# Kernel tuning notes

Hardware: AMD Instinct MI355X
Metric: run time of the kernel (lower is better)

Reference implementation:

```python
import jax, jax.numpy as jnp
import numpy as np

N_NODES = 100000
N_EDGES = 1600000
D_IN, D_HID, D_OUT = 128, 128, 64


def setup_inputs() -> dict:
    key = jax.random.key(0)
    ks = jax.random.split(key, 6)
    x = jax.random.normal(ks[0], (N_NODES, D_IN), dtype=jnp.float32)
    edge_index = jax.random.randint(ks[1], (2, N_EDGES), 0, N_NODES, dtype=jnp.int64)
    s1 = 1.0 / np.sqrt(D_IN)
    s2 = 1.0 / np.sqrt(D_HID)
    return {
        "x": x,
        "edge_index": edge_index,
        "Wl1": jax.random.uniform(ks[2], (D_HID, D_IN), jnp.float32, -s1, s1),
        "bl1": jnp.zeros((D_HID,), jnp.float32),
        "Wr1": jax.random.uniform(ks[3], (D_HID, D_IN), jnp.float32, -s1, s1),
        "Wl2": jax.random.uniform(ks[4], (D_OUT, D_HID), jnp.float32, -s2, s2),
        "bl2": jnp.zeros((D_OUT,), jnp.float32),
        "Wr2": jax.random.uniform(ks[5], (D_OUT, D_HID), jnp.float32, -s2, s2),
    }


def _sage_conv(x, src, dst, Wl, bl, Wr, n_nodes):
    # mean-aggregate neighbor features src -> dst
    agg = jax.ops.segment_sum(x[src], dst, num_segments=n_nodes)  # [N, d_in]
    deg = jax.ops.segment_sum(jnp.ones((src.shape[0],), x.dtype), dst, num_segments=n_nodes)
    agg = agg / jnp.maximum(deg, 1.0)[:, None]
    # PyG SAGEConv: lin_l(agg) + lin_r(x), bias only on lin_l
    return agg @ Wl.T + bl + x @ Wr.T


def reference(x, edge_index, Wl1, bl1, Wr1, Wl2, bl2, Wr2):
    src, dst = edge_index[0], edge_index[1]
    n = x.shape[0]
    h = _sage_conv(x, src, dst, Wl1, bl1, Wr1, n)
    h = jax.nn.relu(h)
    # dropout is identity in eval mode (training=False)
    out = _sage_conv(h, src, dst, Wl2, bl2, Wr2, n)
    return out
```

## Files before the change

### kernel.cpp

```cpp
#include <hip/hip_runtime.h>

#define N_NODES_C 100000
#define N_EDGES_C 1600000
#define NT32_C 3125
#define NBUCK_C 392
#define BCAP_C 4800
#define EPB_C 2048
#define EORD_CAP_C 1536

typedef _Float16 half_t;
typedef __attribute__((ext_vector_type(2))) _Float16 half2v;
typedef __attribute__((ext_vector_type(8))) _Float16 half8v;
typedef __attribute__((ext_vector_type(4))) float floatx4;

#if defined(__has_builtin)
#if __has_builtin(__builtin_amdgcn_fdot2)
#define HAS_FDOT2 1
#endif
#endif

__launch_bounds__(512, 1)
__global__ void bucket_kernel(const int* __restrict__ src, const int* __restrict__ dst,
                              int* __restrict__ gcur, int* __restrict__ bucket, int E) {
    __shared__ int stage[EPB_C];
    __shared__ unsigned short ebkt[EPB_C];
    __shared__ int eord[EPB_C];
    __shared__ unsigned short obkt[EPB_C];
    __shared__ int lcnt[512];
    __shared__ int lcur[512];
    __shared__ int lbase[512];
    __shared__ int sc[2][512];
    const int tid = threadIdx.x;
    const int e0 = blockIdx.x * EPB_C;
    const int n = min(EPB_C, E - e0);

    lcnt[tid] = 0;
    lcur[tid] = 0;
    __syncthreads();
    for (int i = tid; i < n; i += 512) {
        int d = dst[e0 + i];
        int s = src[e0 + i];
        int b = d >> 8;
        stage[i] = (s << 8) | (d & 255);
        ebkt[i] = (unsigned short)b;
        atomicAdd(&lcnt[b], 1);
    }
    __syncthreads();
    sc[0][tid] = lcnt[tid];
    __syncthreads();
    int cur = 0;
    for (int off = 1; off < 512; off <<= 1) {
        int v = sc[cur][tid] + ((tid >= off) ? sc[cur][tid - off] : 0);
        sc[1 - cur][tid] = v;
        __syncthreads();
        cur ^= 1;
    }
    for (int i = tid; i < NBUCK_C; i += 512) {
        int c = lcnt[i];
        lbase[i] = (c > 0) ? atomicAdd(&gcur[i], c) : 0;
    }
    __syncthreads();
    for (int i = tid; i < n; i += 512) {
        int b = ebkt[i];
        int slot = atomicAdd(&lcur[b], 1);
        int pos = (sc[cur][b] - lcnt[b]) + slot;
        eord[pos] = stage[i];
        obkt[pos] = (unsigned short)b;
    }
    __syncthreads();
    for (int i = tid; i < n; i += 512) {
        int b = obkt[i];
        int pre = sc[cur][b] - lcnt[b];
        int gpos = lbase[b] + (i - pre);
        if (gpos < BCAP_C) bucket[b * BCAP_C + gpos] = eord[i];
    }
}

__global__ void scanb_kernel(const int* __restrict__ gcur, int* __restrict__ bbase) {
    __shared__ int sc[2][512];
    const int tid = threadIdx.x;
    int v = (tid < NBUCK_C) ? min(gcur[tid], BCAP_C) : 0;
    sc[0][tid] = v;
    __syncthreads();
    int cur = 0;
    for (int off = 1; off < 512; off <<= 1) {
        int nv = sc[cur][tid] + ((tid >= off) ? sc[cur][tid - off] : 0);
        sc[1 - cur][tid] = nv;
        __syncthreads();
        cur ^= 1;
    }
    if (tid < NBUCK_C) bbase[tid] = sc[cur][tid] - v;
}

__global__ void csr_build_kernel(const int* __restrict__ gcur, const int* __restrict__ bbase,
                                 const int* __restrict__ bucket,
                                 int2* __restrict__ nodeinfo, int* __restrict__ csr, int N) {
    __shared__ int stage[BCAP_C];
    __shared__ int lcnt[256];
    __shared__ int lcur[64];
    __shared__ int sc[2][256];
    __shared__ int eord[EORD_CAP_C];
    const int b = blockIdx.x >> 2;
    const int r = blockIdx.x & 3;
    const int tid = threadIdx.x;
    const int ne = min(gcur[b], BCAP_C);

    lcnt[tid] = 0;
    if (tid < 64) lcur[tid] = 0;
    const int* be = bucket + b * BCAP_C;
    __syncthreads();
    for (int i = tid; i < ne; i += 256) {
        int p = be[i];
        stage[i] = p;
        atomicAdd(&lcnt[p & 255], 1);
    }
    __syncthreads();
    sc[0][tid] = lcnt[tid];
    __syncthreads();
    int cur = 0;
    for (int off = 1; off < 256; off <<= 1) {
        int v = sc[cur][tid] + ((tid >= off) ? sc[cur][tid - off] : 0);
        sc[1 - cur][tid] = v;
        __syncthreads();
        cur ^= 1;
    }
    const int j0 = r * 64;
    const int pre0 = (j0 == 0) ? 0 : sc[cur][j0 - 1];
    const int L = min(sc[cur][j0 + 63] - pre0, EORD_CAP_C);
    for (int i = tid; i < ne; i += 256) {
        int p = stage[i];
        int j = p & 255;
        if ((j >> 6) == r) {
            int slot = atomicAdd(&lcur[j - j0], 1);
            int idx = (sc[cur][j] - lcnt[j]) - pre0 + slot;
            if (idx < EORD_CAP_C) eord[idx] = p >> 8;
        }
    }
    __syncthreads();
    const int gb = bbase[b] + pre0;
    for (int i = tid; i < L; i += 256) csr[gb + i] = eord[i];
    if (tid < 64) {
        int node = (b << 8) + j0 + tid;
        if (node < N) {
            int j = j0 + tid;
            nodeinfo[node] = make_int2(bbase[b] + (sc[cur][j] - lcnt[j]), lcnt[j]);
        }
    }
}

__global__ void prep_kernel(const float* __restrict__ Wl1, const float* __restrict__ Wr1,
                            const float* __restrict__ Wl2, const float* __restrict__ Wr2,
                            const float* __restrict__ x,
                            half_t* __restrict__ B1, half_t* __restrict__ B2,
                            half_t* __restrict__ xh) {
    int blk = blockIdx.x;
    int tid = threadIdx.x;
    if (blk < 128) {
        int t = blk * 256 + tid;
        int j  = t & 7;
        int l  = (t >> 3) & 63;
        int ks = (t >> 9) & 7;
        int ct = t >> 12;
        int k = ks * 32 + ((l >> 4) << 3) + j;
        int o = ct * 16 + (l & 15);
        float v = (k < 128) ? Wl1[o * 128 + k] : Wr1[o * 128 + (k - 128)];
        B1[t] = (half_t)v;
    } else if (blk < 192) {
        int t = (blk - 128) * 256 + tid;
        int j  = t & 7;
        int l  = (t >> 3) & 63;
        int ks = (t >> 9) & 3;
        int ct = t >> 11;
        int k = ks * 32 + ((l >> 4) << 3) + j;
        int o = ct * 16 + (l & 15);
        float v = (o < 64) ? Wl2[o * 128 + k] : Wr2[(o - 64) * 128 + k];
        B2[t] = (half_t)v;
    } else {
        int t = (blk - 192) * 256 + tid;
        if (t >= N_NODES_C * 16) return;
        const float4* p = (const float4*)x;
        float4 a = p[(size_t)t * 2];
        float4 b = p[(size_t)t * 2 + 1];
        half_t r[8] = {(half_t)a.x, (half_t)a.y, (half_t)a.z, (half_t)a.w,
                       (half_t)b.x, (half_t)b.y, (half_t)b.z, (half_t)b.w};
        *(uint4*)(xh + (size_t)t * 8) = *(uint4*)r;
    }
}

static __device__ __forceinline__ void dot8(float* a, uint4 v) {
    unsigned int u[4] = {v.x, v.y, v.z, v.w};
#ifdef HAS_FDOT2
    const half2v e0 = {(half_t)1.0f, (half_t)0.0f};
    const half2v e1 = {(half_t)0.0f, (half_t)1.0f};
#pragma unroll
    for (int i = 0; i < 4; i++) {
        union { unsigned int x; half2v h; } c; c.x = u[i];
        a[2 * i]     = __builtin_amdgcn_fdot2(c.h, e0, a[2 * i], false);
        a[2 * i + 1] = __builtin_amdgcn_fdot2(c.h, e1, a[2 * i + 1], false);
    }
#else
#pragma unroll
    for (int i = 0; i < 4; i++) {
        union { unsigned int x; half2v h; } c; c.x = u[i];
        a[2 * i]     += (float)c.h.x;
        a[2 * i + 1] += (float)c.h.y;
    }
#endif
}

__launch_bounds__(256, 2)
__global__ void l1_kernel(const half_t* __restrict__ xh,
                          const int2* __restrict__ nodeinfo,
                          const int* __restrict__ csr,
                          const half_t* __restrict__ B1,
                          const float* __restrict__ bias,
                          half_t* __restrict__ hh) {
    __shared__ half_t sA[32][264];

    const int wave = threadIdx.x >> 6;
    const int lane = threadIdx.x & 63;
    const int quad = lane >> 4;
    const int l16 = lane & 15;
    const int tid = threadIdx.x;
    const int node0 = blockIdx.x * 32;

    for (int u = tid; u < 512; u += 256) {
        int n = u >> 4, cc = u & 15;
        *(half8v*)&sA[n][128 + cc * 8] =
            *(const half8v*)(xh + (size_t)(node0 + n) * 128 + cc * 8);
    }

    for (int i = 0; i < 8; i++) {
        const int n = wave * 8 + i;
        const int2 info = nodeinfo[node0 + n];
        const int* row = csr + info.x;
        const int deg = info.y;
        float a0[8] = {0,0,0,0,0,0,0,0};
        float a1[8] = {0,0,0,0,0,0,0,0};
        int e = quad;
        for (; e + 4 < deg; e += 8) {
            int s0 = row[e];
            int s1 = row[e + 4];
            uint4 v0 = *(const uint4*)(xh + (size_t)s0 * 128 + l16 * 8);
            uint4 v1 = *(const uint4*)(xh + (size_t)s1 * 128 + l16 * 8);
            dot8(a0, v0);
            dot8(a1, v1);
        }
        if (e < deg) {
            uint4 v0 = *(const uint4*)(xh + (size_t)row[e] * 128 + l16 * 8);
            dot8(a0, v0);
        }
        float sc = 1.0f / fmaxf((float)deg, 1.0f);
#pragma unroll
        for (int j = 0; j < 8; j++) {
            float v = a0[j] + a1[j];
            v += __shfl_xor(v, 16, 64);
            v += __shfl_xor(v, 32, 64);
            a0[j] = v * sc;
        }
        if (lane < 16) {
            half_t r[8];
#pragma unroll
            for (int j = 0; j < 8; j++) r[j] = (half_t)a0[j];
            *(uint4*)&sA[n][l16 * 8] = *(uint4*)r;
        }
    }
    __syncthreads();

    half8v bf[2][8];
    float bias_v[2];
#pragma unroll
    for (int i = 0; i < 2; i++) {
        int ct = wave * 2 + i;
        bias_v[i] = bias[ct * 16 + l16];
#pragma unroll
        for (int ks = 0; ks < 8; ks++) {
            bf[i][ks] = *(const half8v*)(B1 + ((ct * 8 + ks) * 64 + lane) * 8);
        }
    }

    floatx4 acc[2][2];
#pragma unroll
    for (int i = 0; i < 2; i++)
#pragma unroll
        for (int s = 0; s < 2; s++)
            acc[i][s] = (floatx4){0.f, 0.f, 0.f, 0.f};

#pragma unroll
    for (int ks = 0; ks < 8; ks++) {
        half8v a0 = *(const half8v*)&sA[l16][ks * 32 + quad * 8];
        half8v a1 = *(const half8v*)&sA[16 + l16][ks * 32 + quad * 8];
#pragma unroll
        for (int i = 0; i < 2; i++) {
            acc[i][0] = __builtin_amdgcn_mfma_f32_16x16x32_f16(a0, bf[i][ks], acc[i][0], 0, 0, 0);
            acc[i][1] = __builtin_amdgcn_mfma_f32_16x16x32_f16(a1, bf[i][ks], acc[i][1], 0, 0, 0);
        }
    }

#pragma unroll
    for (int i = 0; i < 2; i++) {
        int o = wave * 32 + i * 16 + l16;
#pragma unroll
        for (int s = 0; s < 2; s++) {
            float vals[4] = {acc[i][s].x, acc[i][s].y, acc[i][s].z, acc[i][s].w};
#pragma unroll
            for (int r = 0; r < 4; r++) {
                int node = node0 + s * 16 + quad * 4 + r;
                float v = fmaxf(vals[r] + bias_v[i], 0.f);
                hh[(size_t)node * 128 + o] = (half_t)v;
            }
        }
    }
}

__launch_bounds__(256, 2)
__global__ void gemm2_kernel(const half_t* __restrict__ hh,
                             const half_t* __restrict__ B2,
                             const float* __restrict__ bias,
                             half_t* __restrict__ g,
                             half_t* __restrict__ s2h) {
    __shared__ half_t sA[32][136];

    const int wave = threadIdx.x >> 6;
    const int lane = threadIdx.x & 63;
    const int quad = lane >> 4;
    const int l16 = lane & 15;

    half8v bf[2][4];
    float bias_v[2];
#pragma unroll
    for (int i = 0; i < 2; i++) {
        int ct = wave * 2 + i;
        int o = ct * 16 + l16;
        bias_v[i] = (o >= 64) ? bias[o - 64] : 0.f;
#pragma unroll
        for (int ks = 0; ks < 4; ks++) {
            bf[i][ks] = *(const half8v*)(B2 + ((ct * 4 + ks) * 64 + lane) * 8);
        }
    }

    const int tid = threadIdx.x;

    for (int tile = blockIdx.x; tile < NT32_C; tile += gridDim.x) {
        const int node0 = tile * 32;
        for (int u = tid; u < 512; u += 256) {
            int n = u >> 4, cc = u & 15;
            *(half8v*)&sA[n][cc * 8] =
                *(const half8v*)(hh + (size_t)(node0 + n) * 128 + cc * 8);
        }
        __syncthreads();

        floatx4 acc[2][2];
#pragma unroll
        for (int i = 0; i < 2; i++)
#pragma unroll
            for (int s = 0; s < 2; s++)
                acc[i][s] = (floatx4){0.f, 0.f, 0.f, 0.f};

#pragma unroll
        for (int ks = 0; ks < 4; ks++) {
            half8v a0 = *(const half8v*)&sA[l16][ks * 32 + quad * 8];
            half8v a1 = *(const half8v*)&sA[16 + l16][ks * 32 + quad * 8];
#pragma unroll
            for (int i = 0; i < 2; i++) {
                acc[i][0] = __builtin_amdgcn_mfma_f32_16x16x32_f16(a0, bf[i][ks], acc[i][0], 0, 0, 0);
                acc[i][1] = __builtin_amdgcn_mfma_f32_16x16x32_f16(a1, bf[i][ks], acc[i][1], 0, 0, 0);
            }
        }

#pragma unroll
        for (int i = 0; i < 2; i++) {
            int o = wave * 32 + i * 16 + l16;
#pragma unroll
            for (int s = 0; s < 2; s++) {
                float vals[4] = {acc[i][s].x, acc[i][s].y, acc[i][s].z, acc[i][s].w};
#pragma unroll
                for (int r = 0; r < 4; r++) {
                    int node = node0 + s * 16 + quad * 4 + r;
                    float v = vals[r] + bias_v[i];
                    if (o < 64) g[(size_t)node * 64 + o] = (half_t)v;
                    else        s2h[(size_t)node * 64 + (o - 64)] = (half_t)v;
                }
            }
        }
        __syncthreads();
    }
}

__global__ void agg2e_kernel(const half_t* __restrict__ g,
                             const half_t* __restrict__ s2h,
                             const int2* __restrict__ nodeinfo,
                             const int* __restrict__ csr,
                             float* __restrict__ out, int N) {
    int wid = (blockIdx.x * 256 + threadIdx.x) >> 6;
    if (wid >= N) return;
    int lane = threadIdx.x & 63;
    int q = lane >> 3;
    int c = lane & 7;
    int2 info = nodeinfo[wid];
    const int* row = csr + info.x;
    const int deg = info.y;
    float a0[8] = {0,0,0,0,0,0,0,0};
    float a1[8] = {0,0,0,0,0,0,0,0};
    int e = q;
    for (; e + 8 < deg; e += 16) {
        int s0 = row[e];
        int s1 = row[e + 8];
        uint4 v0 = *(const uint4*)(g + (size_t)s0 * 64 + c * 8);
        uint4 v1 = *(const uint4*)(g + (size_t)s1 * 64 + c * 8);
        dot8(a0, v0);
        dot8(a1, v1);
    }
    if (e < deg) {
        uint4 v0 = *(const uint4*)(g + (size_t)row[e] * 64 + c * 8);
        dot8(a0, v0);
    }
    float acc[8];
#pragma unroll
    for (int j = 0; j < 8; j++) {
        float v = a0[j] + a1[j];
        v += __shfl_xor(v, 8, 64);
        v += __shfl_xor(v, 16, 64);
        v += __shfl_xor(v, 32, 64);
        acc[j] = v;
    }
    if (lane < 8) {
        float sc = 1.0f / fmaxf((float)deg, 1.0f);
        uint4 sv = *(const uint4*)(s2h + (size_t)wid * 64 + c * 8);
        union { unsigned int x; half2v h; } c0, c1, c2, c3;
        c0.x = sv.x; c1.x = sv.y; c2.x = sv.z; c3.x = sv.w;
        float4 r0, r1;
        r0.x = acc[0] * sc + (float)c0.h.x;
        r0.y = acc[1] * sc + (float)c0.h.y;
        r0.z = acc[2] * sc + (float)c1.h.x;
        r0.w = acc[3] * sc + (float)c1.h.y;
        r1.x = acc[4] * sc + (float)c2.h.x;
        r1.y = acc[5] * sc + (float)c2.h.y;
        r1.z = acc[6] * sc + (float)c3.h.x;
        r1.w = acc[7] * sc + (float)c3.h.y;
        *(float4*)(out + (size_t)wid * 64 + c * 8) = r0;
        *(float4*)(out + (size_t)wid * 64 + c * 8 + 4) = r1;
    }
}

extern "C" void kernel_launch(void* const* d_in, const int* in_sizes, int n_in,
                              void* d_out, int out_size, void* d_ws, size_t ws_size,
                              hipStream_t stream) {
    const float* x    = (const float*)d_in[0];
    const int*   ei   = (const int*)d_in[1];
    const float* Wl1  = (const float*)d_in[2];
    const float* bl1  = (const float*)d_in[3];
    const float* Wr1  = (const float*)d_in[4];
    const float* Wl2  = (const float*)d_in[5];
    const float* bl2  = (const float*)d_in[6];
    const float* Wr2  = (const float*)d_in[7];
    float* out = (float*)d_out;

    const int N = N_NODES_C;
    const int E = N_EDGES_C;
    const int* src = ei;
    const int* dst = ei + E;

    char* ws = (char*)d_ws;
    half_t* B1   = (half_t*)(ws + 0);
    half_t* B2   = (half_t*)(ws + 65536);
    int*    gcur = (int*)   (ws + 98304);
    int*    bbase= (int*)   (ws + 100352);
    int2*   nodeinfo = (int2*)(ws + 102400);
    int*    csr  = (int*)   (ws + 1048576);
    half_t* xh   = (half_t*)(ws + 7448576);
    half_t* aggh = (half_t*)(ws + 33048576);
    half_t* hh   = (half_t*)(ws + 58648576);
    half_t* g    = aggh;
    half_t* s2h  = aggh + 6400000;
    int*    bucket = (int*)hh;

    hipMemsetAsync(gcur, 0, NBUCK_C * sizeof(int), stream);
    bucket_kernel<<<(E + EPB_C - 1) / EPB_C, 512, 0, stream>>>(src, dst, gcur, bucket, E);
    scanb_kernel<<<1, 512, 0, stream>>>(gcur, bbase);
    csr_build_kernel<<<NBUCK_C * 4, 256, 0, stream>>>(gcur, bbase, bucket, nodeinfo, csr, N);

    prep_kernel<<<192 + (N * 16 + 255) / 256, 256, 0, stream>>>(
        Wl1, Wr1, Wl2, Wr2, x, B1, B2, xh);

    l1_kernel<<<NT32_C, 256, 0, stream>>>(xh, nodeinfo, csr, B1, bl1, hh);

    gemm2_kernel<<<512, 256, 0, stream>>>(hh, B2, bl2, g, s2h);
    agg2e_kernel<<<(N + 3) / 4, 256, 0, stream>>>(g, s2h, nodeinfo, csr, out, N);
}
```

Measured before the change: 278.5 us.

## Split layer-1 gather into wave-per-node kernel and fuse both GEMMs

Layer-1 aggregation moves out of the combined l1 kernel into a separate one-wave-per-node gather kernel that unrolls the edge loop 4x and writes the mean-aggregated features to a buffer. Both dense layers then run in one persistent MFMA kernel, with the ReLU hidden tile kept in shared memory, so the hidden activations are never written to global memory. The bucket-prefix scan is folded into csr_build (each block redoes the 392-entry scan), and the memset is folded into prep_kernel, cutting two launches. In exchange the aggregated features take an extra global write and read, and the fused GEMM kernel holds more registers for both weight sets.

```diff
diff --git a/kernel.cpp b/kernel.cpp
--- a/kernel.cpp
+++ b/kernel.cpp
@@ -76,11 +76,23 @@
     }
 }
 
-__global__ void scanb_kernel(const int* __restrict__ gcur, int* __restrict__ bbase) {
+__launch_bounds__(512, 1)
+__global__ void csr_build_kernel(const int* __restrict__ gcur, const int* __restrict__ bucket,
+                                 int2* __restrict__ nodeinfo, int* __restrict__ csr, int N) {
+    __shared__ int stage[BCAP_C];
+    __shared__ int lcnt[256];
+    __shared__ int lcur[64];
     __shared__ int sc[2][512];
+    __shared__ int eord[EORD_CAP_C];
+    __shared__ int bbase_s;
+    const int b = blockIdx.x >> 2;
+    const int r = blockIdx.x & 3;
     const int tid = threadIdx.x;
+
     int v = (tid < NBUCK_C) ? min(gcur[tid], BCAP_C) : 0;
     sc[0][tid] = v;
+    if (tid < 256) lcnt[tid] = 0;
+    if (tid < 64) lcur[tid] = 0;
     __syncthreads();
     int cur = 0;
     for (int off = 1; off < 512; off <<= 1) {
@@ -89,45 +101,30 @@
         __syncthreads();
         cur ^= 1;
     }
-    if (tid < NBUCK_C) bbase[tid] = sc[cur][tid] - v;
-}
-
-__global__ void csr_build_kernel(const int* __restrict__ gcur, const int* __restrict__ bbase,
-                                 const int* __restrict__ bucket,
-                                 int2* __restrict__ nodeinfo, int* __restrict__ csr, int N) {
-    __shared__ int stage[BCAP_C];
-    __shared__ int lcnt[256];
-    __shared__ int lcur[64];
-    __shared__ int sc[2][256];
-    __shared__ int eord[EORD_CAP_C];
-    const int b = blockIdx.x >> 2;
-    const int r = blockIdx.x & 3;
-    const int tid = threadIdx.x;
+    if (tid == 0) bbase_s = (b == 0) ? 0 : sc[cur][b - 1];
     const int ne = min(gcur[b], BCAP_C);
-
-    lcnt[tid] = 0;
-    if (tid < 64) lcur[tid] = 0;
     const int* be = bucket + b * BCAP_C;
     __syncthreads();
-    for (int i = tid; i < ne; i += 256) {
+
+    for (int i = tid; i < ne; i += 512) {
         int p = be[i];
         stage[i] = p;
         atomicAdd(&lcnt[p & 255], 1);
     }
     __syncthreads();
-    sc[0][tid] = lcnt[tid];
-    __syncthreads();
-    int cur = 0;
+    sc[0][tid] = (tid < 256) ? lcnt[tid] : 0;
+    __syncthreads();
+    cur = 0;
     for (int off = 1; off < 256; off <<= 1) {
-        int v = sc[cur][tid] + ((tid >= off) ? sc[cur][tid - off] : 0);
-        sc[1 - cur][tid] = v;
+        int nv = sc[cur][tid] + ((tid >= off) ? sc[cur][tid - off] : 0);
+        sc[1 - cur][tid] = nv;
         __syncthreads();
         cur ^= 1;
     }
     const int j0 = r * 64;
     const int pre0 = (j0 == 0) ? 0 : sc[cur][j0 - 1];
     const int L = min(sc[cur][j0 + 63] - pre0, EORD_CAP_C);
-    for (int i = tid; i < ne; i += 256) {
+    for (int i = tid; i < ne; i += 512) {
         int p = stage[i];
         int j = p & 255;
         if ((j >> 6) == r) {
@@ -137,13 +134,13 @@
         }
     }
     __syncthreads();
-    const int gb = bbase[b] + pre0;
-    for (int i = tid; i < L; i += 256) csr[gb + i] = eord[i];
+    const int gb = bbase_s + pre0;
+    for (int i = tid; i < L; i += 512) csr[gb + i] = eord[i];
     if (tid < 64) {
         int node = (b << 8) + j0 + tid;
         if (node < N) {
             int j = j0 + tid;
-            nodeinfo[node] = make_int2(bbase[b] + (sc[cur][j] - lcnt[j]), lcnt[j]);
+            nodeinfo[node] = make_int2(bbase_s + (sc[cur][j] - lcnt[j]), lcnt[j]);
         }
     }
 }
@@ -152,9 +149,10 @@
                             const float* __restrict__ Wl2, const float* __restrict__ Wr2,
                             const float* __restrict__ x,
                             half_t* __restrict__ B1, half_t* __restrict__ B2,
-                            half_t* __restrict__ xh) {
+                            half_t* __restrict__ xh, int* __restrict__ gcur) {
     int blk = blockIdx.x;
     int tid = threadIdx.x;
+    if (blk == 0 && tid < 196) { gcur[tid] = 0; gcur[tid + 196] = 0; }
     if (blk < 128) {
         int t = blk * 256 + tid;
         int j  = t & 7;
@@ -208,145 +206,108 @@
 #endif
 }
 
+__global__ void agg1_kernel(const half_t* __restrict__ xh,
+                            const int2* __restrict__ nodeinfo,
+                            const int* __restrict__ csr,
+                            half_t* __restrict__ aggh, int N) {
+    int wid = (blockIdx.x * 256 + threadIdx.x) >> 6;
+    if (wid >= N) return;
+    int lane = threadIdx.x & 63;
+    int q = lane >> 4;
+    int c = lane & 15;
+    int2 info = nodeinfo[wid];
+    const int* row = csr + info.x;
+    const int deg = info.y;
+    float a0[8] = {0,0,0,0,0,0,0,0};
+    float a1[8] = {0,0,0,0,0,0,0,0};
+    int e = q;
+    for (; e + 12 < deg; e += 16) {
+        int s0 = row[e];
+        int s1 = row[e + 4];
+        int s2 = row[e + 8];
+        int s3 = row[e + 12];
+        uint4 v0 = *(const uint4*)(xh + (size_t)s0 * 128 + c * 8);
+        uint4 v1 = *(const uint4*)(xh + (size_t)s1 * 128 + c * 8);
+        uint4 v2 = *(const uint4*)(xh + (size_t)s2 * 128 + c * 8);
+        uint4 v3 = *(const uint4*)(xh + (size_t)s3 * 128 + c * 8);
+        dot8(a0, v0);
+        dot8(a1, v1);
+        dot8(a0, v2);
+        dot8(a1, v3);
+    }
+    for (; e + 4 < deg; e += 8) {
+        int s0 = row[e];
+        int s1 = row[e + 4];
+        uint4 v0 = *(const uint4*)(xh + (size_t)s0 * 128 + c * 8);
+        uint4 v1 = *(const uint4*)(xh + (size_t)s1 * 128 + c * 8);
+        dot8(a0, v0);
+        dot8(a1, v1);
+    }
+    if (e < deg) {
+        uint4 v0 = *(const uint4*)(xh + (size_t)row[e] * 128 + c * 8);
+        dot8(a0, v0);
+    }
+    float acc[8];
+#pragma unroll
+    for (int j = 0; j < 8; j++) {
+        float v = a0[j] + a1[j];
+        v += __shfl_xor(v, 16, 64);
+        v += __shfl_xor(v, 32, 64);
+        acc[j] = v;
+    }
+    if (lane < 16) {
+        float sc = 1.0f / fmaxf((float)deg, 1.0f);
+        half_t r[8];
+#pragma unroll
+        for (int j = 0; j < 8; j++) r[j] = (half_t)(acc[j] * sc);
+        *(uint4*)(aggh + (size_t)wid * 128 + c * 8) = *(uint4*)r;
+    }
+}
+
 __launch_bounds__(256, 2)
-__global__ void l1_kernel(const half_t* __restrict__ xh,
-                          const int2* __restrict__ nodeinfo,
-                          const int* __restrict__ csr,
-                          const half_t* __restrict__ B1,
-                          const float* __restrict__ bias,
-                          half_t* __restrict__ hh) {
+__global__ void gemm12_kernel(const half_t* __restrict__ aggh,
+                              const half_t* __restrict__ xh,
+                              const half_t* __restrict__ B1,
+                              const float* __restrict__ bias1,
+                              const half_t* __restrict__ B2,
+                              const float* __restrict__ bias2,
+                              half_t* __restrict__ g,
+                              half_t* __restrict__ s2h) {
     __shared__ half_t sA[32][264];
+    __shared__ half_t sH[32][136];
 
     const int wave = threadIdx.x >> 6;
     const int lane = threadIdx.x & 63;
     const int quad = lane >> 4;
     const int l16 = lane & 15;
     const int tid = threadIdx.x;
-    const int node0 = blockIdx.x * 32;
-
-    for (int u = tid; u < 512; u += 256) {
-        int n = u >> 4, cc = u & 15;
-        *(half8v*)&sA[n][128 + cc * 8] =
-            *(const half8v*)(xh + (size_t)(node0 + n) * 128 + cc * 8);
-    }
-
-    for (int i = 0; i < 8; i++) {
-        const int n = wave * 8 + i;
-        const int2 info = nodeinfo[node0 + n];
-        const int* row = csr + info.x;
-        const int deg = info.y;
-        float a0[8] = {0,0,0,0,0,0,0,0};
-        float a1[8] = {0,0,0,0,0,0,0,0};
-        int e = quad;
-        for (; e + 4 < deg; e += 8) {
-            int s0 = row[e];
-            int s1 = row[e + 4];
-            uint4 v0 = *(const uint4*)(xh + (size_t)s0 * 128 + l16 * 8);
-            uint4 v1 = *(const uint4*)(xh + (size_t)s1 * 128 + l16 * 8);
-            dot8(a0, v0);
-            dot8(a1, v1);
-        }
-        if (e < deg) {
-            uint4 v0 = *(const uint4*)(xh + (size_t)row[e] * 128 + l16 * 8);
-            dot8(a0, v0);
-        }
-        float sc = 1.0f / fmaxf((float)deg, 1.0f);
-#pragma unroll
-        for (int j = 0; j < 8; j++) {
-            float v = a0[j] + a1[j];
-            v += __shfl_xor(v, 16, 64);
-            v += __shfl_xor(v, 32, 64);
-            a0[j] = v * sc;
-        }
-        if (lane < 16) {
-            half_t r[8];
-#pragma unroll
-            for (int j = 0; j < 8; j++) r[j] = (half_t)a0[j];
-            *(uint4*)&sA[n][l16 * 8] = *(uint4*)r;
-        }
-    }
-    __syncthreads();
-
-    half8v bf[2][8];
-    float bias_v[2];
+
+    half8v bf1[2][8];
+    float bv1[2];
+    half8v bf2[2][4];
+    float bv2[2];
 #pragma unroll
     for (int i = 0; i < 2; i++) {
         int ct = wave * 2 + i;
-        bias_v[i] = bias[ct * 16 + l16];
-#pragma unroll
-        for (int ks = 0; ks < 8; ks++) {
-            bf[i][ks] = *(const half8v*)(B1 + ((ct * 8 + ks) * 64 + lane) * 8);
-        }
-    }
-
-    floatx4 acc[2][2];
-#pragma unroll
-    for (int i = 0; i < 2; i++)
-#pragma unroll
-        for (int s = 0; s < 2; s++)
-            acc[i][s] = (floatx4){0.f, 0.f, 0.f, 0.f};
-
-#pragma unroll
-    for (int ks = 0; ks < 8; ks++) {
-        half8v a0 = *(const half8v*)&sA[l16][ks * 32 + quad * 8];
-        half8v a1 = *(const half8v*)&sA[16 + l16][ks * 32 + quad * 8];
-#pragma unroll
-        for (int i = 0; i < 2; i++) {
-            acc[i][0] = __builtin_amdgcn_mfma_f32_16x16x32_f16(a0, bf[i][ks], acc[i][0], 0, 0, 0);
-            acc[i][1] = __builtin_amdgcn_mfma_f32_16x16x32_f16(a1, bf[i][ks], acc[i][1], 0, 0, 0);
-        }
-    }
-
-#pragma unroll
-    for (int i = 0; i < 2; i++) {
-        int o = wave * 32 + i * 16 + l16;
-#pragma unroll
-        for (int s = 0; s < 2; s++) {
-            float vals[4] = {acc[i][s].x, acc[i][s].y, acc[i][s].z, acc[i][s].w};
-#pragma unroll
-            for (int r = 0; r < 4; r++) {
-                int node = node0 + s * 16 + quad * 4 + r;
-                float v = fmaxf(vals[r] + bias_v[i], 0.f);
-                hh[(size_t)node * 128 + o] = (half_t)v;
-            }
-        }
-    }
-}
-
-__launch_bounds__(256, 2)
-__global__ void gemm2_kernel(const half_t* __restrict__ hh,
-                             const half_t* __restrict__ B2,
-                             const float* __restrict__ bias,
-                             half_t* __restrict__ g,
-                             half_t* __restrict__ s2h) {
-    __shared__ half_t sA[32][136];
-
-    const int wave = threadIdx.x >> 6;
-    const int lane = threadIdx.x & 63;
-    const int quad = lane >> 4;
-    const int l16 = lane & 15;
-
-    half8v bf[2][4];
-    float bias_v[2];
-#pragma unroll
-    for (int i = 0; i < 2; i++) {
-        int ct = wave * 2 + i;
+        bv1[i] = bias1[ct * 16 + l16];
         int o = ct * 16 + l16;
-        bias_v[i] = (o >= 64) ? bias[o - 64] : 0.f;
-#pragma unroll
-        for (int ks = 0; ks < 4; ks++) {
-            bf[i][ks] = *(const half8v*)(B2 + ((ct * 4 + ks) * 64 + lane) * 8);
-        }
-    }
-
-    const int tid = threadIdx.x;
+        bv2[i] = (o >= 64) ? bias2[o - 64] : 0.f;
+#pragma unroll
+        for (int ks = 0; ks < 8; ks++)
+            bf1[i][ks] = *(const half8v*)(B1 + ((ct * 8 + ks) * 64 + lane) * 8);
+#pragma unroll
+        for (int ks = 0; ks < 4; ks++)
+            bf2[i][ks] = *(const half8v*)(B2 + ((ct * 4 + ks) * 64 + lane) * 8);
+    }
 
     for (int tile = blockIdx.x; tile < NT32_C; tile += gridDim.x) {
         const int node0 = tile * 32;
         for (int u = tid; u < 512; u += 256) {
             int n = u >> 4, cc = u & 15;
             *(half8v*)&sA[n][cc * 8] =
-                *(const half8v*)(hh + (size_t)(node0 + n) * 128 + cc * 8);
+                *(const half8v*)(aggh + (size_t)(node0 + n) * 128 + cc * 8);
+            *(half8v*)&sA[n][128 + cc * 8] =
+                *(const half8v*)(xh + (size_t)(node0 + n) * 128 + cc * 8);
         }
         __syncthreads();
 
@@ -356,18 +317,16 @@
 #pragma unroll
             for (int s = 0; s < 2; s++)
                 acc[i][s] = (floatx4){0.f, 0.f, 0.f, 0.f};
-
-#pragma unroll
-        for (int ks = 0; ks < 4; ks++) {
+#pragma unroll
+        for (int ks = 0; ks < 8; ks++) {
             half8v a0 = *(const half8v*)&sA[l16][ks * 32 + quad * 8];
             half8v a1 = *(const half8v*)&sA[16 + l16][ks * 32 + quad * 8];
 #pragma unroll
             for (int i = 0; i < 2; i++) {
-                acc[i][0] = __builtin_amdgcn_mfma_f32_16x16x32_f16(a0, bf[i][ks], acc[i][0], 0, 0, 0);
-                acc[i][1] = __builtin_amdgcn_mfma_f32_16x16x32_f16(a1, bf[i][ks], acc[i][1], 0, 0, 0);
+                acc[i][0] = __builtin_amdgcn_mfma_f32_16x16x32_f16(a0, bf1[i][ks], acc[i][0], 0, 0, 0);
+                acc[i][1] = __builtin_amdgcn_mfma_f32_16x16x32_f16(a1, bf1[i][ks], acc[i][1], 0, 0, 0);
             }
         }
-
 #pragma unroll
         for (int i = 0; i < 2; i++) {
             int o = wave * 32 + i * 16 + l16;
@@ -376,8 +335,38 @@
                 float vals[4] = {acc[i][s].x, acc[i][s].y, acc[i][s].z, acc[i][s].w};
 #pragma unroll
                 for (int r = 0; r < 4; r++) {
+                    int n = s * 16 + quad * 4 + r;
+                    sH[n][o] = (half_t)fmaxf(vals[r] + bv1[i], 0.f);
+                }
+            }
+        }
+        __syncthreads();
+
+#pragma unroll
+        for (int i = 0; i < 2; i++)
+#pragma unroll
+            for (int s = 0; s < 2; s++)
+                acc[i][s] = (floatx4){0.f, 0.f, 0.f, 0.f};
+#pragma unroll
+        for (int ks = 0; ks < 4; ks++) {
+            half8v a0 = *(const half8v*)&sH[l16][ks * 32 + quad * 8];
+            half8v a1 = *(const half8v*)&sH[16 + l16][ks * 32 + quad * 8];
+#pragma unroll
+            for (int i = 0; i < 2; i++) {
+                acc[i][0] = __builtin_amdgcn_mfma_f32_16x16x32_f16(a0, bf2[i][ks], acc[i][0], 0, 0, 0);
+                acc[i][1] = __builtin_amdgcn_mfma_f32_16x16x32_f16(a1, bf2[i][ks], acc[i][1], 0, 0, 0);
+            }
+        }
+#pragma unroll
+        for (int i = 0; i < 2; i++) {
+            int o = wave * 32 + i * 16 + l16;
+#pragma unroll
+            for (int s = 0; s < 2; s++) {
+                float vals[4] = {acc[i][s].x, acc[i][s].y, acc[i][s].z, acc[i][s].w};
+#pragma unroll
+                for (int r = 0; r < 4; r++) {
                     int node = node0 + s * 16 + quad * 4 + r;
-                    float v = vals[r] + bias_v[i];
+                    float v = vals[r] + bv2[i];
                     if (o < 64) g[(size_t)node * 64 + o] = (half_t)v;
                     else        s2h[(size_t)node * 64 + (o - 64)] = (half_t)v;
                 }
@@ -465,26 +454,19 @@
     half_t* B1   = (half_t*)(ws + 0);
     half_t* B2   = (half_t*)(ws + 65536);
     int*    gcur = (int*)   (ws + 98304);
-    int*    bbase= (int*)   (ws + 100352);
     int2*   nodeinfo = (int2*)(ws + 102400);
     int*    csr  = (int*)   (ws + 1048576);
     half_t* xh   = (half_t*)(ws + 7448576);
-    half_t* aggh = (half_t*)(ws + 33048576);
-    half_t* hh   = (half_t*)(ws + 58648576);
-    half_t* g    = aggh;
-    half_t* s2h  = aggh + 6400000;
-    int*    bucket = (int*)hh;
-
-    hipMemsetAsync(gcur, 0, NBUCK_C * sizeof(int), stream);
+    half_t* g    = (half_t*)(ws + 33048576);
+    half_t* s2h  = g + 6400000;
+    half_t* aggh = (half_t*)(ws + 58648576);
+    int*    bucket = (int*)aggh;
+
+    prep_kernel<<<192 + (N * 16 + 255) / 256, 256, 0, stream>>>(
+        Wl1, Wr1, Wl2, Wr2, x, B1, B2, xh, gcur);
     bucket_kernel<<<(E + EPB_C - 1) / EPB_C, 512, 0, stream>>>(src, dst, gcur, bucket, E);
-    scanb_kernel<<<1, 512, 0, stream>>>(gcur, bbase);
-    csr_build_kernel<<<NBUCK_C * 4, 256, 0, stream>>>(gcur, bbase, bucket, nodeinfo, csr, N);
-
-    prep_kernel<<<192 + (N * 16 + 255) / 256, 256, 0, stream>>>(
-        Wl1, Wr1, Wl2, Wr2, x, B1, B2, xh);
-
-    l1_kernel<<<NT32_C, 256, 0, stream>>>(xh, nodeinfo, csr, B1, bl1, hh);
-
-    gemm2_kernel<<<512, 256, 0, stream>>>(hh, B2, bl2, g, s2h);
+    csr_build_kernel<<<NBUCK_C * 4, 512, 0, stream>>>(gcur, bucket, nodeinfo, csr, N);
+    agg1_kernel<<<(N + 3) / 4, 256, 0, stream>>>(xh, nodeinfo, csr, aggh, N);
+    gemm12_kernel<<<512, 256, 0, stream>>>(aggh, xh, B1, bl1, B2, bl2, g, s2h);
     agg2e_kernel<<<(N + 3) / 4, 256, 0, stream>>>(g, s2h, nodeinfo, csr, out, N);
 }
```

Measured after the change: 265.1 us. 1.05x faster.
